# Kernel optimization log

Measured on AMD Instinct MI355X. Metric: run time of the kernel, lower is better.

Reference implementation:

```python
import jax, jax.numpy as jnp
import numpy as np

S, B, C, H, W = 5, 128, 256, 11, 11
HEADS, R, NITER = 8, 2, 2
HD = C // HEADS
SCALE = C ** (-0.5)
EPS = 1e-5


def conv(x, w, b, p=1):
    o = jax.lax.conv_general_dilated(x, w, (1, 1), [(p, p), (p, p)],
                                     dimension_numbers=('NCHW', 'OIHW', 'NCHW'))
    return o + b[None, :, None, None]


def ln(x, g, b):
    # torch LayerNorm over normalized_shape=[C,H,W]
    m = jnp.mean(x, axis=(1, 2, 3), keepdims=True)
    v = jnp.var(x, axis=(1, 2, 3), keepdims=True)
    return (x - m) * jax.lax.rsqrt(v + EPS) * g[None] + b[None]


def setup_inputs():
    ks = iter(jax.random.split(jax.random.key(0), 40))
    def nrm(shp, s=0.02):
        return jax.random.normal(next(ks), shp, jnp.float32) * s
    def c3(o, i):
        return nrm((o, i, 3, 3)), jnp.zeros((o,), jnp.float32)
    d = {}
    d['x'] = jax.random.normal(next(ks), (S, B, C, H, W), jnp.float32)
    d['ing'] = jnp.ones((C, H, W), jnp.float32); d['inb'] = jnp.zeros((C, H, W), jnp.float32)
    d['iqw'], d['iqb'] = c3(C, C); d['ikw'], d['ikb'] = c3(C, C); d['ivw'], d['ivb'] = c3(C, C)
    d['iow'], d['iob'] = c3(C, C)
    d['iong'] = jnp.ones((C, H, W), jnp.float32); d['ionb'] = jnp.zeros((C, H, W), jnp.float32)
    d['ia'] = jnp.array(1.0, jnp.float32)
    d['eng'] = jnp.ones((C, H, W), jnp.float32); d['enb'] = jnp.zeros((C, H, W), jnp.float32)
    d['rpe'] = nrm((2 * R, 1, H, W), 1.0)
    d['mw'], d['mb'] = c3(C, C + 3)  # hidden + 2 temporal + 1 spatial embedding channel
    d['eqw'], d['eqb'] = c3(C, C); d['ekw'], d['ekb'] = c3(C, C); d['evw'], d['evb'] = c3(C, C)
    d['gw'] = nrm((C, 2 * C, 1, 1)); d['gb'] = jnp.zeros((C,), jnp.float32)
    d['eow'], d['eob'] = c3(C, C)
    d['eong'] = jnp.ones((C, H, W), jnp.float32); d['eonb'] = jnp.zeros((C, H, W), jnp.float32)
    d['iia'] = jnp.array(0.5, jnp.float32)
    d['zrw'], d['zrb'] = c3(2 * C, 2 * C)
    d['hw_'], d['hb_'] = c3(C, 2 * C)
    d['ng'] = jnp.ones((C, H, W), jnp.float32); d['nb'] = jnp.zeros((C, H, W), jnp.float32)
    return d


def _forward(x, ing, inb, iqw, iqb, ikw, ikb, ivw, ivb, iow, iob, iong, ionb, ia,
             eng, enb, rpe, mw, mb, eqw, eqb, ekw, ekb, evw, evb, gw, gb,
             eow, eob, eong, eonb, iia, zrw, zrb, hw_, hb_, ng, nb):
    def intra_all(h):
        # intra-frame self-attention, vectorized over all S frames at once
        xf = h.reshape(S * B, C, H, W)
        xn = ln(xf, ing, inb)
        q = conv(xn, iqw, iqb).reshape(S * B, C, H * W)
        k = conv(xn, ikw, ikb).reshape(S * B, C, H * W)
        v = conv(xn, ivw, ivb).reshape(S * B, C, H * W)
        a = jax.nn.softmax(jnp.einsum('bcn,bcm->bnm', q, k) * SCALE, axis=-1)
        o = jnp.einsum('bnm,bcm->bcn', a, v).reshape(S * B, C, H, W)
        o = jax.nn.relu(ln(conv(o, iow, iob), iong, ionb))
        return (ia * o + xn).reshape(S, B, C, H, W)

    def inter_one(i, h):
        xn = ln(h[i], eng, enb)
        q = conv(xn, eqw, eqb).reshape(B, HEADS, HD, H * W)
        out = jnp.zeros((B, C, H, W), jnp.float32)
        for j in range(S):
            if j == i or abs(i - j) > R:
                continue
            idx = (i - j + R - 1) % (2 * R)  # mimics python negative indexing in torch
            tenc = jnp.array([1.0 if i < j else -1.0, abs(i - j) / R], jnp.float32)
            tenc = jnp.broadcast_to(tenc[None, :, None, None], (B, 2, H, W))
            sp = jnp.broadcast_to(rpe[idx][None], (B, 1, H, W))
            y = conv(jnp.concatenate([h[j], tenc, sp], axis=1), mw, mb)
            k = conv(y, ekw, ekb).reshape(B, HEADS, HD, H * W)
            v = conv(y, evw, evb).reshape(B, HEADS, HD, H * W)
            a = jax.nn.softmax(jnp.einsum('bhdn,bhdm->bhnm', q, k) * SCALE, axis=-1)
            msg = jnp.einsum('bhdm,bhnm->bhdn', v, a).reshape(B, C, H, W)
            msg = jax.nn.relu(ln(conv(msg, eow, eob), eong, eonb))
            gate = jax.nn.sigmoid(jnp.mean(conv(jnp.concatenate([xn, msg], axis=1), gw, gb, p=0),
                                           axis=(2, 3), keepdims=True))
            out = out + msg * gate
        return out

    def gru(xin, hprev):
        zr = jax.nn.sigmoid(conv(jnp.concatenate([xin, hprev], axis=1), zrw, zrb))
        z, r = zr[:, :C], zr[:, C:]
        hhat = jnp.tanh(conv(jnp.concatenate([xin, r * hprev], axis=1), hw_, hb_))
        return (1 - z) * hprev + z * hhat

    h = x
    for _ in range(NITER):
        hi = intra_all(h)
        new_h = []
        for i in range(S):
            inter = inter_one(i, h)
            comb = iia * hi[i] + (1 - iia) * inter
            nh = gru(comb, h[i]) + h[i]
            new_h.append(ln(nh, ng, nb))
        h = jnp.stack(new_h, axis=0)
    return h


def reference(x, ing, inb, iqw, iqb, ikw, ikb, ivw, ivb, iow, iob, iong, ionb, ia,
              eng, enb, rpe, mw, mb, eqw, eqb, ekw, ekb, evw, evb, gw, gb,
              eow, eob, eong, eonb, iia, zrw, zrb, hw_, hb_, ng, nb):
    return _forward(x, ing, inb, iqw, iqb, ikw, ikb, ivw, ivb, iow, iob, iong, ionb, ia,
                    eng, enb, rpe, mw, mb, eqw, eqb, ekw, ekb, evw, evb, gw, gb,
                    eow, eob, eong, eonb, iia, zrw, zrb, hw_, hb_, ng, nb)
```

## Files before the change

kernel.cpp:

```cpp
#include <hip/hip_runtime.h>
#include <cstdint>
#include <cstddef>
#include <cmath>


#define Sn 5
#define Bn 128
#define Cn 256
#define Nn 121
#define HEADSn 8
#define NITERn 2
#define EPSf 1e-5f
#define SCALEf 0.0625f
#define CHWn (Cn*Nn)

static const size_t SLICEsz = (size_t)Bn*CHWn;
static const size_t FULLsz  = (size_t)Sn*SLICEsz;
static const size_t SLA     = SLICEsz + 1024;

typedef __attribute__((ext_vector_type(8))) short short8;
typedef __attribute__((ext_vector_type(4))) float f32x4;

static __device__ __forceinline__ short f2bf(float f){
  union { float f; unsigned u; } x; x.f = f;
  unsigned r = (x.u + 0x7FFFu + ((x.u >> 16) & 1u)) >> 16;
  return (short)r;
}

__global__ __launch_bounds__(128) void wprep_kernel(
    const float* __restrict__ w, short* __restrict__ o, int Cin, int Cinp)
{
  const int co = blockIdx.x, tap = blockIdx.y;
  const int G = Cinp >> 7;
  const int coH = co >> 6, ms = (co >> 4) & 3, l15 = co & 15;
  const float* wrow = w + (size_t)co*Cin*9 + tap;
  short* obase = o + (size_t)coH*G*73728 + (size_t)tap*8192 + ms*512 + l15*8;
  for (int ci = threadIdx.x; ci < Cinp; ci += 128){
    const int grp = ci >> 7, kc = (ci >> 5) & 3, quad = (ci >> 3) & 3, e = ci & 7;
    const short val = (ci < Cin) ? f2bf(wrow[(size_t)ci*9]) : (short)0;
    obase[(size_t)grp*73728 + kc*2048 + quad*128 + e] = val;
  }
}

__global__ __launch_bounds__(256) void gwt_kernel(
    const float* __restrict__ gw, float* __restrict__ gwT)
{
  const int k = blockIdx.x, c = threadIdx.x;
  gwT[(size_t)k*256 + c] = gw[(size_t)c*512 + k];
}

__global__ __launch_bounds__(512) void conv_mfma_kernel(
    const float* __restrict__ inA, const float* __restrict__ inA1,
    const float* __restrict__ inB,
    int cinA, int Cin, int Cinp, int Cout,
    const short* __restrict__ wbf, const float* __restrict__ bias,
    float* __restrict__ out,
    int mMode, float4 tcs,
    const float* __restrict__ rp0, const float* __restrict__ rp1)
{
  __shared__ short Xs[128*136];
  const int samp = blockIdx.x;
  const int coB  = blockIdx.y * 128;
  const int t    = threadIdx.x;
  const int lane = t & 63;
  const int wv   = t >> 6;
  const int wy   = wv >> 2;
  const int wx   = wv & 3;
  const int l15  = lane & 15;
  const int quad = lane >> 4;
  const int G    = Cinp >> 7;

  const int pr = samp >> 7;
  const float* baseA = inA1 ? ((pr ? inA1 : inA) + (size_t)(samp & 127)*cinA*Nn)
                            : (inA + (size_t)samp*(size_t)cinA*Nn);
  const float* baseB = inB ? inB + (size_t)samp*(size_t)(Cin-cinA)*Nn : nullptr;
  const float mtc0 = pr ? tcs.z : tcs.x;
  const float mtc1 = pr ? tcs.w : tcs.y;
  const float* rp  = pr ? rp1 : rp0;

  int nout[2], py[2], pxx[2];
  #pragma unroll
  for (int ns = 0; ns < 2; ++ns){
    nout[ns] = wx*32 + ns*16 + l15;
    py[ns]  = nout[ns] / 11;
    pxx[ns] = nout[ns] % 11;
  }

  f32x4 acc[4][2];
  #pragma unroll
  for (int ms = 0; ms < 4; ++ms)
    #pragma unroll
    for (int ns = 0; ns < 2; ++ns) acc[ms][ns] = (f32x4){0.f,0.f,0.f,0.f};

  const short* wgbase = wbf + (size_t)(blockIdx.y*2 + wy)*G*73728 + lane*8;

  const int ngrp = (Cin + 127) >> 7;
  for (int grp = 0; grp < ngrp; ++grp){
    __syncthreads();
    for (int e = t; e < 128*128; e += 512){
      const int px = e & 127, cil = e >> 7;
      const int ci = grp*128 + cil;
      float v = 0.f;
      if (px < Nn && ci < Cin){
        if (mMode && ci >= 256)
          v = (ci == 256) ? mtc0 : (ci == 257) ? mtc1 : rp[px];
        else if (ci < cinA) v = baseA[(size_t)ci*Nn + px];
        else                v = baseB[(size_t)(ci-cinA)*Nn + px];
      }
      Xs[px*136 + cil] = f2bf(v);
    }
    __syncthreads();

    const int rem = Cin - grp*128;
    const short* wgrp = wgbase + (size_t)grp*73728;

    if (rem >= 128){
      for (int tap = 0; tap < 9; ++tap){
        const int dy = tap/3 - 1, dx = tap%3 - 1;
        int pp[2];
        #pragma unroll
        for (int ns = 0; ns < 2; ++ns){
          const int yy = py[ns] + dy, xx = pxx[ns] + dx;
          const bool ok = (nout[ns] < Nn) && yy >= 0 && yy < 11 && xx >= 0 && xx < 11;
          pp[ns] = ok ? yy*11 + xx : Nn;
        }
        const short* wb = wgrp + tap*8192;
        #pragma unroll
        for (int kc = 0; kc < 4; ++kc){
          short8 a[4], b[2];
          #pragma unroll
          for (int ms = 0; ms < 4; ++ms)
            a[ms] = *(const short8*)(wb + kc*2048 + ms*512);
          #pragma unroll
          for (int ns = 0; ns < 2; ++ns)
            b[ns] = *(const short8*)(&Xs[pp[ns]*136 + kc*32 + quad*8]);
          #pragma unroll
          for (int ms = 0; ms < 4; ++ms)
            #pragma unroll
            for (int ns = 0; ns < 2; ++ns)
              acc[ms][ns] = __builtin_amdgcn_mfma_f32_16x16x32_bf16(
                                a[ms], b[ns], acc[ms][ns], 0, 0, 0);
        }
      }
    } else {
      const int nkc = (rem + 31) >> 5;
      for (int tap = 0; tap < 9; ++tap){
        const int dy = tap/3 - 1, dx = tap%3 - 1;
        int pp[2];
        #pragma unroll
        for (int ns = 0; ns < 2; ++ns){
          const int yy = py[ns] + dy, xx = pxx[ns] + dx;
          const bool ok = (nout[ns] < Nn) && yy >= 0 && yy < 11 && xx >= 0 && xx < 11;
          pp[ns] = ok ? yy*11 + xx : Nn;
        }
        const short* wb = wgrp + tap*8192;
        for (int kc = 0; kc < nkc; ++kc){
          short8 a[4], b[2];
          #pragma unroll
          for (int ms = 0; ms < 4; ++ms)
            a[ms] = *(const short8*)(wb + kc*2048 + ms*512);
          #pragma unroll
          for (int ns = 0; ns < 2; ++ns)
            b[ns] = *(const short8*)(&Xs[pp[ns]*136 + kc*32 + quad*8]);
          #pragma unroll
          for (int ms = 0; ms < 4; ++ms)
            #pragma unroll
            for (int ns = 0; ns < 2; ++ns)
              acc[ms][ns] = __builtin_amdgcn_mfma_f32_16x16x32_bf16(
                                a[ms], b[ns], acc[ms][ns], 0, 0, 0);
        }
      }
    }
  }

  #pragma unroll
  for (int ms = 0; ms < 4; ++ms)
    #pragma unroll
    for (int ns = 0; ns < 2; ++ns){
      const int n = nout[ns];
      if (n < Nn){
        const int mbase = coB + wy*64 + ms*16 + quad*4;
        #pragma unroll
        for (int r = 0; r < 4; ++r)
          out[((size_t)samp*Cout + mbase + r)*Nn + n] = acc[ms][ns][r] + bias[mbase + r];
      }
    }
}

__global__ __launch_bounds__(256) void ln_kernel(
    const float* __restrict__ x, const float* __restrict__ g, const float* __restrict__ bb,
    float* __restrict__ out, const float* __restrict__ alpha,
    const float* __restrict__ addend, int relu)
{
  const size_t base = (size_t)blockIdx.x * CHWn;
  const f32x4* xs = (const f32x4*)(x + base);
  const int NV = CHWn/4;
  float sum = 0.f, ss = 0.f;
  for (int i = threadIdx.x; i < NV; i += 256){
    f32x4 v = xs[i];
    sum += v.x + v.y + v.z + v.w;
    ss  += v.x*v.x + v.y*v.y + v.z*v.z + v.w*v.w;
  }
  #pragma unroll
  for (int o = 32; o > 0; o >>= 1){ sum += __shfl_down(sum, o, 64); ss += __shfl_down(ss, o, 64); }
  __shared__ float r1[4], r2[4];
  const int wid = threadIdx.x >> 6;
  if ((threadIdx.x & 63) == 0){ r1[wid] = sum; r2[wid] = ss; }
  __syncthreads();
  sum = r1[0]+r1[1]+r1[2]+r1[3];
  ss  = r2[0]+r2[1]+r2[2]+r2[3];
  const float mean = sum * (1.f/CHWn);
  const float var  = ss * (1.f/CHWn) - mean*mean;
  const float inv  = rsqrtf(var + EPSf);
  const float a = alpha ? *alpha : 1.f;
  const f32x4* gv = (const f32x4*)g;
  const f32x4* bv = (const f32x4*)bb;
  const f32x4* av = addend ? (const f32x4*)(addend + base) : nullptr;
  f32x4* ov = (f32x4*)(out + base);
  for (int i = threadIdx.x; i < NV; i += 256){
    f32x4 v = (xs[i] - mean) * inv * gv[i] + bv[i];
    if (relu){ v.x=fmaxf(v.x,0.f); v.y=fmaxf(v.y,0.f); v.z=fmaxf(v.z,0.f); v.w=fmaxf(v.w,0.f); }
    v *= a;
    if (av) v += av[i];
    ov[i] = v;
  }
}

template<int HDt, int CPT, int NPASS>
__global__ __launch_bounds__(256) void attn_kernel(
    const float* __restrict__ q, const float* __restrict__ k, const float* __restrict__ v,
    float* __restrict__ o, int qs, int ks, int os, int qm)
{
  __shared__ float T[Nn*132];
  const int nh_ = Cn / HDt;
  const int samp = blockIdx.x / nh_;
  const int hh = blockIdx.x % nh_;
  const size_t qoff  = ((size_t)(samp & qm)*qs + hh*HDt)*Nn;
  const size_t kvoff = ((size_t)samp*ks + hh*HDt)*Nn;
  const size_t ooff  = ((size_t)samp*os + hh*HDt)*Nn;
  const int t = threadIdx.x;
  {
    const int tn = t >> 4, tm = t & 15;
    const int n0 = tn*8, m0 = tm*8;
    float acc[8][8];
    #pragma unroll
    for (int a2=0;a2<8;a2++)
      #pragma unroll
      for (int b2=0;b2<8;b2++) acc[a2][b2] = 0.f;
    const float* qp = q + qoff + n0;
    const float* kp = k + kvoff + m0;
    #pragma unroll 2
    for (int d=0; d<HDt; ++d){
      float qv[8], kv[8];
      #pragma unroll
      for (int j2=0;j2<8;j2++){ qv[j2] = qp[d*Nn + j2]; kv[j2] = kp[d*Nn + j2]; }
      #pragma unroll
      for (int a2=0;a2<8;a2++)
        #pragma unroll
        for (int b2=0;b2<8;b2++) acc[a2][b2] = fmaf(qv[a2], kv[b2], acc[a2][b2]);
    }
    #pragma unroll
    for (int b2=0;b2<8;b2++){
      const int m = m0 + b2;
      if (m < Nn){
        #pragma unroll
        for (int a2=0;a2<8;a2++) T[m*132 + n0 + a2] = acc[a2][b2] * SCALEf;
      }
    }
  }
  __syncthreads();
  if (t < Nn){
    float mx = -1e30f;
    for (int m2=0;m2<Nn;m2++) mx = fmaxf(mx, T[m2*132+t]);
    float sum = 0.f;
    for (int m2=0;m2<Nn;m2++){ float e = __expf(T[m2*132+t]-mx); sum += e; T[m2*132+t] = e; }
    const float invs = 1.f/sum;
    for (int m2=0;m2<Nn;m2++) T[m2*132+t] *= invs;
  }
  __syncthreads();
  {
    const int ng_ = t & 15, cg = t >> 4;
    const int an0 = ng_*8;
    for (int pass=0; pass<NPASS; ++pass){
      const int c0 = pass*64 + cg*CPT;
      float av[CPT][8];
      #pragma unroll
      for (int ci2=0;ci2<CPT;ci2++)
        #pragma unroll
        for (int j2=0;j2<8;j2++) av[ci2][j2] = 0.f;
      for (int m2=0;m2<Nn;m2++){
        float tv[8];
        #pragma unroll
        for (int j2=0;j2<8;j2++) tv[j2] = T[m2*132 + an0 + j2];
        #pragma unroll
        for (int ci2=0;ci2<CPT;ci2++){
          const float vv = v[kvoff + (size_t)(c0+ci2)*Nn + m2];
          #pragma unroll
          for (int j2=0;j2<8;j2++) av[ci2][j2] = fmaf(vv, tv[j2], av[ci2][j2]);
        }
      }
      #pragma unroll
      for (int ci2=0;ci2<CPT;ci2++){
        float* op = o + ooff + (size_t)(c0+ci2)*Nn + an0;
        #pragma unroll
        for (int j2=0;j2<8;j2++) if (an0+j2 < Nn) op[j2] = av[ci2][j2];
      }
    }
  }
}

__global__ __launch_bounds__(128) void mean_kernel(const float* __restrict__ x, float* __restrict__ out)
{
  const int s = blockIdx.x; const int c0 = blockIdx.y*8;
  __shared__ float r[2];
  for (int cc=0; cc<8; ++cc){
    const int c = c0+cc;
    float v = 0.f;
    if (threadIdx.x < Nn) v = x[((size_t)s*Cn + c)*Nn + threadIdx.x];
    #pragma unroll
    for (int o=32;o>0;o>>=1) v += __shfl_down(v, o, 64);
    if ((threadIdx.x & 63) == 0) r[threadIdx.x>>6] = v;
    __syncthreads();
    if (threadIdx.x == 0) out[(size_t)s*Cn + c] = (r[0]+r[1]) * (1.f/Nn);
    __syncthreads();
  }
}

__global__ __launch_bounds__(256) void gate_kernel(
    const float* __restrict__ meanX, const float* __restrict__ meanM,
    const float* __restrict__ gwT, const float* __restrict__ gb,
    float* __restrict__ gate, int xm)
{
  const int b = blockIdx.x;
  __shared__ float mv[512];
  mv[threadIdx.x]     = meanX[(size_t)(b & xm)*Cn + threadIdx.x];
  mv[256+threadIdx.x] = meanM[(size_t)b*Cn + threadIdx.x];
  __syncthreads();
  float acc = gb[threadIdx.x];
  for (int k2=0;k2<512;k2++) acc = fmaf(gwT[(size_t)k2*256 + threadIdx.x], mv[k2], acc);
  gate[(size_t)b*Cn + threadIdx.x] = 1.f/(1.f+__expf(-acc));
}

__global__ __launch_bounds__(256) void accum_kernel(
    const float* __restrict__ msg, const float* __restrict__ gate,
    float* __restrict__ outs, int init)
{
  const size_t idx = (size_t)blockIdx.x*256 + threadIdx.x;
  if (idx >= SLICEsz) return;
  const size_t t_ = idx / Nn;
  const int c = (int)(t_ & 255);
  const int b = (int)(t_ >> 8);
  const float v = msg[idx] * gate[(size_t)b*Cn + c];
  outs[idx] = init ? v : (outs[idx] + v);
}

__global__ __launch_bounds__(256) void comb_kernel(float* __restrict__ hi,
    const float* __restrict__ outi, const float* __restrict__ iia)
{
  const size_t idx = (size_t)blockIdx.x*256 + threadIdx.x;
  if (idx >= SLICEsz) return;
  const float a = *iia;
  hi[idx] = a*hi[idx] + (1.f-a)*outi[idx];
}

__global__ __launch_bounds__(256) void rh_kernel(const float* __restrict__ zrq,
    const float* __restrict__ h, float* __restrict__ rh, size_t nelem)
{
  const size_t idx = (size_t)blockIdx.x*256 + threadIdx.x;
  if (idx >= nelem) return;
  const int n_ = (int)(idx % Nn);
  const size_t t_ = idx / Nn;
  const int c = (int)(t_ & 255);
  const size_t s = t_ >> 8;
  float r = zrq[(s*512 + 256 + c)*Nn + n_];
  r = 1.f/(1.f+__expf(-r));
  rh[idx] = r*h[idx];
}

__global__ __launch_bounds__(256) void nh_kernel(const float* __restrict__ zrq,
    const float* __restrict__ hq, const float* __restrict__ h,
    float* __restrict__ nh, size_t nelem)
{
  const size_t idx = (size_t)blockIdx.x*256 + threadIdx.x;
  if (idx >= nelem) return;
  const int n_ = (int)(idx % Nn);
  const size_t t_ = idx / Nn;
  const int c = (int)(t_ & 255);
  const size_t s = t_ >> 8;
  float z = zrq[(s*512 + c)*Nn + n_];
  z = 1.f/(1.f+__expf(-z));
  const float hv = h[idx];
  nh[idx] = (1.f-z)*hv + z*tanhf(hq[idx]) + hv;
}

static const int PJ[5][4] = {{1,2,0,0},{0,2,3,0},{0,1,3,4},{1,2,4,0},{2,3,0,0}};
static const int PNP[5]   = {2,3,4,3,2};

extern "C" void kernel_launch(void* const* d_in, const int* in_sizes, int n_in,
                              void* d_out, int out_size, void* d_ws, size_t ws_size,
                              hipStream_t stream)
{
  (void)in_sizes; (void)n_in; (void)out_size;
  const float* x   = (const float*)d_in[0];
  const float* ing = (const float*)d_in[1];
  const float* inb = (const float*)d_in[2];
  const float* iqw = (const float*)d_in[3];
  const float* iqb = (const float*)d_in[4];
  const float* ikw = (const float*)d_in[5];
  const float* ikb = (const float*)d_in[6];
  const float* ivw = (const float*)d_in[7];
  const float* ivb = (const float*)d_in[8];
  const float* iow = (const float*)d_in[9];
  const float* iob = (const float*)d_in[10];
  const float* iong= (const float*)d_in[11];
  const float* ionb= (const float*)d_in[12];
  const float* ia  = (const float*)d_in[13];
  const float* eng = (const float*)d_in[14];
  const float* enb = (const float*)d_in[15];
  const float* rpe = (const float*)d_in[16];
  const float* mw  = (const float*)d_in[17];
  const float* mb  = (const float*)d_in[18];
  const float* eqw = (const float*)d_in[19];
  const float* eqb = (const float*)d_in[20];
  const float* ekw = (const float*)d_in[21];
  const float* ekb = (const float*)d_in[22];
  const float* evw = (const float*)d_in[23];
  const float* evb = (const float*)d_in[24];
  const float* gw  = (const float*)d_in[25];
  const float* gb  = (const float*)d_in[26];
  const float* eow = (const float*)d_in[27];
  const float* eob = (const float*)d_in[28];
  const float* eong= (const float*)d_in[29];
  const float* eonb= (const float*)d_in[30];
  const float* iia = (const float*)d_in[31];
  const float* zrw = (const float*)d_in[32];
  const float* zrb = (const float*)d_in[33];
  const float* hww = (const float*)d_in[34];
  const float* hwb = (const float*)d_in[35];
  const float* ng  = (const float*)d_in[36];
  const float* nbg = (const float*)d_in[37];

  float* W = (float*)d_ws;
  size_t off = 0;
  float* h      = W + off; off += FULLsz + 1024;
  float* big    = W + off; off += 6*SLICEsz + 1024;
  float* p2     = W + off; off += 2*SLICEsz + 1024;
  float* xsl    = W + off; off += 2*SLICEsz + 1024;
  float* qsl    = W + off; off += SLA;
  float* osl    = W + off; off += SLA;
  float* meanXb = W + off; off += Bn*Cn;
  float* meanM  = W + off; off += 2*Bn*Cn;
  float* gateb  = W + off; off += 2*Bn*Cn;
  float* bqkv   = W + off; off += 768;
  float* bekv   = W + off; off += 512;
  float* gwT    = W + off; off += 512*256;
  short* WB = (short*)(W + off);
  size_t so = 0;
  short* iqB = WB + so; so += (size_t)256*9*256;
  short* ikB = WB + so; so += (size_t)256*9*256;
  short* ivB = WB + so; so += (size_t)256*9*256;
  short* ioB = WB + so; so += (size_t)256*9*256;
  short* eqB = WB + so; so += (size_t)256*9*256;
  short* ekB = WB + so; so += (size_t)256*9*256;
  short* evB = WB + so; so += (size_t)256*9*256;
  short* eoB = WB + so; so += (size_t)256*9*256;
  short* mB_ = WB + so; so += (size_t)256*9*384;
  short* zrB = WB + so; so += (size_t)512*9*512;
  short* hwB = WB + so; so += (size_t)256*9*512;
  off += (so + 1) / 2;
  if (ws_size < off * sizeof(float)) return;

  float* hi = (float*)d_out;

  hipMemcpyAsync(h, x, FULLsz*sizeof(float), hipMemcpyDeviceToDevice, stream);
  hipMemcpyAsync(bqkv,     iqb, 256*sizeof(float), hipMemcpyDeviceToDevice, stream);
  hipMemcpyAsync(bqkv+256, ikb, 256*sizeof(float), hipMemcpyDeviceToDevice, stream);
  hipMemcpyAsync(bqkv+512, ivb, 256*sizeof(float), hipMemcpyDeviceToDevice, stream);
  hipMemcpyAsync(bekv,     ekb, 256*sizeof(float), hipMemcpyDeviceToDevice, stream);
  hipMemcpyAsync(bekv+256, evb, 256*sizeof(float), hipMemcpyDeviceToDevice, stream);

  wprep_kernel<<<dim3(256,9),128,0,stream>>>(iqw, iqB, 256, 256);
  wprep_kernel<<<dim3(256,9),128,0,stream>>>(ikw, ikB, 256, 256);
  wprep_kernel<<<dim3(256,9),128,0,stream>>>(ivw, ivB, 256, 256);
  wprep_kernel<<<dim3(256,9),128,0,stream>>>(iow, ioB, 256, 256);
  wprep_kernel<<<dim3(256,9),128,0,stream>>>(eqw, eqB, 256, 256);
  wprep_kernel<<<dim3(256,9),128,0,stream>>>(ekw, ekB, 256, 256);
  wprep_kernel<<<dim3(256,9),128,0,stream>>>(evw, evB, 256, 256);
  wprep_kernel<<<dim3(256,9),128,0,stream>>>(eow, eoB, 256, 256);
  wprep_kernel<<<dim3(256,9),128,0,stream>>>(mw,  mB_, 259, 384);
  wprep_kernel<<<dim3(512,9),128,0,stream>>>(zrw, zrB, 512, 512);
  wprep_kernel<<<dim3(256,9),128,0,stream>>>(hww, hwB, 512, 512);
  gwt_kernel<<<512,256,0,stream>>>(gw, gwT);

  const int gridSlc = (int)(SLICEsz / 256);
  const float4 f4z = {0.f,0.f,0.f,0.f};

  #define CONV(inA_, inB_, Cin_, Cinp_, Cout_, wb_, bi_, out_, NS_)              \
    conv_mfma_kernel<<<dim3(Bn*(NS_), (Cout_)/128), 512, 0, stream>>>(           \
        inA_, nullptr, inB_, 256, Cin_, Cinp_, Cout_, wb_, bi_, out_,            \
        0, f4z, nullptr, nullptr)

  for (int it = 0; it < NITERn; ++it){
    for (int s0 = 0; s0 < Sn; s0 += 2){
      const int cn = (Sn - s0 >= 2) ? 2 : 1;
      const float* hs = h + (size_t)s0*SLICEsz;
      ln_kernel<<<Bn*cn,256,0,stream>>>(hs, ing, inb, xsl, nullptr, nullptr, 0);
      CONV(xsl, nullptr, 256, 256, 768, iqB, bqkv, big, cn);
      attn_kernel<256,4,4><<<Bn*cn,256,0,stream>>>(big, big + (size_t)256*Nn,
                                                big + (size_t)512*Nn, p2,
                                                768, 768, 256, 0x7fffffff);
      CONV(p2, nullptr, 256, 256, 256, ioB, iob, big, cn);
      ln_kernel<<<Bn*cn,256,0,stream>>>(big, iong, ionb, hi + (size_t)s0*SLICEsz, ia, xsl, 1);
    }

    for (int i = 0; i < Sn; ++i){
      ln_kernel<<<Bn,256,0,stream>>>(h + (size_t)i*SLICEsz, eng, enb, xsl, nullptr, nullptr, 0);
      CONV(xsl, nullptr, 256, 256, 256, eqB, eqb, qsl, 1);
      mean_kernel<<<dim3(Bn,32),128,0,stream>>>(xsl, meanXb);
      const int np = PNP[i];
      int done = 0; int first = 1;
      while (done < np){
        const int cn = (np - done >= 2) ? 2 : 1;
        const int j0 = PJ[i][done];
        const int j1 = PJ[i][done + cn - 1];
        const float4 tcs = { (i < j0) ? 1.f : -1.f, fabsf((float)(i - j0)) * 0.5f,
                             (i < j1) ? 1.f : -1.f, fabsf((float)(i - j1)) * 0.5f };
        const int r0 = (((i - j0 + 1) % 4) + 4) % 4;
        const int r1 = (((i - j1 + 1) % 4) + 4) % 4;
        conv_mfma_kernel<<<dim3(Bn*cn,2),512,0,stream>>>(
            h + (size_t)j0*SLICEsz, h + (size_t)j1*SLICEsz, nullptr,
            256, 259, 384, 256, mB_, mb, big,
            1, tcs, rpe + (size_t)r0*Nn, rpe + (size_t)r1*Nn);
        CONV(big, nullptr, 256, 256, 512, ekB, bekv, big + 2*SLICEsz, cn);
        attn_kernel<32,2,1><<<Bn*cn*HEADSn,256,0,stream>>>(
            qsl, big + 2*SLICEsz, big + 2*SLICEsz + (size_t)256*Nn, big,
            256, 512, 256, 127);
        CONV(big, nullptr, 256, 256, 256, eoB, eob, p2, cn);
        ln_kernel<<<Bn*cn,256,0,stream>>>(p2, eong, eonb, p2, nullptr, nullptr, 1);
        mean_kernel<<<dim3(Bn*cn,32),128,0,stream>>>(p2, meanM);
        gate_kernel<<<Bn*cn,256,0,stream>>>(meanXb, meanM, gwT, gb, gateb, 127);
        accum_kernel<<<gridSlc,256,0,stream>>>(p2, gateb, osl, first);
        if (cn == 2)
          accum_kernel<<<gridSlc,256,0,stream>>>(p2 + SLICEsz, gateb + Bn*Cn, osl, 0);
        first = 0; done += cn;
      }
      comb_kernel<<<gridSlc,256,0,stream>>>(hi + (size_t)i*SLICEsz, osl, iia);
    }

    for (int s0 = 0; s0 < Sn; s0 += 2){
      const int cn = (Sn - s0 >= 2) ? 2 : 1;
      const float* hs = h + (size_t)s0*SLICEsz;
      float* cs = hi + (size_t)s0*SLICEsz;
      CONV(cs, hs, 512, 512, 512, zrB, zrb, big, cn);
      rh_kernel<<<gridSlc*cn,256,0,stream>>>(big, hs, xsl, (size_t)cn*SLICEsz);
      CONV(cs, xsl, 512, 512, 256, hwB, hwb, p2, cn);
      nh_kernel<<<gridSlc*cn,256,0,stream>>>(big, p2, hs, xsl, (size_t)cn*SLICEsz);
      float* dst = (it == NITERn-1) ? cs : (float*)hs;
      ln_kernel<<<Bn*cn,256,0,stream>>>(xsl, ng, nbg, dst, nullptr, nullptr, 0);
    }
  }
  #undef CONV
}
```

Baseline: 14.25 ms.

## Batch inter-frame pairs across frames in fixed pairs, fold comb into accumulate

```diff
diff --git a/kernel.cpp b/kernel.cpp
--- a/kernel.cpp
+++ b/kernel.cpp
@@ -16,7 +16,6 @@
 
 static const size_t SLICEsz = (size_t)Bn*CHWn;
 static const size_t FULLsz  = (size_t)Sn*SLICEsz;
-static const size_t SLA     = SLICEsz + 1024;
 
 typedef __attribute__((ext_vector_type(8))) short short8;
 typedef __attribute__((ext_vector_type(4))) float f32x4;
@@ -229,13 +228,18 @@
 template<int HDt, int CPT, int NPASS>
 __global__ __launch_bounds__(256) void attn_kernel(
     const float* __restrict__ q, const float* __restrict__ k, const float* __restrict__ v,
-    float* __restrict__ o, int qs, int ks, int os, int qm)
+    float* __restrict__ o, int qs, int ks, int os, int qsel0, int qsel1)
 {
   __shared__ float T[Nn*132];
   const int nh_ = Cn / HDt;
   const int samp = blockIdx.x / nh_;
   const int hh = blockIdx.x % nh_;
-  const size_t qoff  = ((size_t)(samp & qm)*qs + hh*HDt)*Nn;
+  size_t qoff;
+  if (qsel0 < 0) qoff = ((size_t)samp*qs + hh*HDt)*Nn;
+  else {
+    const int slot = (samp >> 7) ? qsel1 : qsel0;
+    qoff = ((size_t)slot*Bn + (samp & 127))*(size_t)CHWn + (size_t)hh*HDt*Nn;
+  }
   const size_t kvoff = ((size_t)samp*ks + hh*HDt)*Nn;
   const size_t ooff  = ((size_t)samp*os + hh*HDt)*Nn;
   const int t = threadIdx.x;
@@ -329,11 +333,12 @@
 __global__ __launch_bounds__(256) void gate_kernel(
     const float* __restrict__ meanX, const float* __restrict__ meanM,
     const float* __restrict__ gwT, const float* __restrict__ gb,
-    float* __restrict__ gate, int xm)
+    float* __restrict__ gate, int xi0, int xi1)
 {
   const int b = blockIdx.x;
+  const int xi = (b >> 7) ? xi1 : xi0;
   __shared__ float mv[512];
-  mv[threadIdx.x]     = meanX[(size_t)(b & xm)*Cn + threadIdx.x];
+  mv[threadIdx.x]     = meanX[((size_t)xi*Bn + (b & 127))*Cn + threadIdx.x];
   mv[256+threadIdx.x] = meanM[(size_t)b*Cn + threadIdx.x];
   __syncthreads();
   float acc = gb[threadIdx.x];
@@ -343,24 +348,16 @@
 
 __global__ __launch_bounds__(256) void accum_kernel(
     const float* __restrict__ msg, const float* __restrict__ gate,
-    float* __restrict__ outs, int init)
+    float* __restrict__ hi, const float* __restrict__ iia, int init)
 {
   const size_t idx = (size_t)blockIdx.x*256 + threadIdx.x;
   if (idx >= SLICEsz) return;
   const size_t t_ = idx / Nn;
   const int c = (int)(t_ & 255);
   const int b = (int)(t_ >> 8);
-  const float v = msg[idx] * gate[(size_t)b*Cn + c];
-  outs[idx] = init ? v : (outs[idx] + v);
-}
-
-__global__ __launch_bounds__(256) void comb_kernel(float* __restrict__ hi,
-    const float* __restrict__ outi, const float* __restrict__ iia)
-{
-  const size_t idx = (size_t)blockIdx.x*256 + threadIdx.x;
-  if (idx >= SLICEsz) return;
   const float a = *iia;
-  hi[idx] = a*hi[idx] + (1.f-a)*outi[idx];
+  const float w = (1.f - a) * msg[idx] * gate[(size_t)b*Cn + c];
+  hi[idx] = init ? (a*hi[idx] + w) : (hi[idx] + w);
 }
 
 __global__ __launch_bounds__(256) void rh_kernel(const float* __restrict__ zrq,
@@ -393,8 +390,9 @@
   nh[idx] = (1.f-z)*hv + z*tanhf(hq[idx]) + hv;
 }
 
-static const int PJ[5][4] = {{1,2,0,0},{0,2,3,0},{0,1,3,4},{1,2,4,0},{2,3,0,0}};
-static const int PNP[5]   = {2,3,4,3,2};
+static const int PIg[14] = {0,0,1,1,1,2,2,2,2,3,3,3,4,4};
+static const int PJg[14] = {1,2,0,2,3,0,1,3,4,1,2,4,2,3};
+static const int FIRSTP[5] = {0,2,5,9,12};
 
 extern "C" void kernel_launch(void* const* d_in, const int* in_sizes, int n_in,
                               void* d_out, int out_size, void* d_ws, size_t ws_size,
@@ -446,9 +444,8 @@
   float* big    = W + off; off += 6*SLICEsz + 1024;
   float* p2     = W + off; off += 2*SLICEsz + 1024;
   float* xsl    = W + off; off += 2*SLICEsz + 1024;
-  float* qsl    = W + off; off += SLA;
-  float* osl    = W + off; off += SLA;
-  float* meanXb = W + off; off += Bn*Cn;
+  float* qsl    = W + off; off += 2*SLICEsz + 1024;
+  float* meanXb = W + off; off += 2*Bn*Cn;
   float* meanM  = W + off; off += 2*Bn*Cn;
   float* gateb  = W + off; off += 2*Bn*Cn;
   float* bqkv   = W + off; off += 768;
@@ -500,6 +497,16 @@
         inA_, nullptr, inB_, 256, Cin_, Cinp_, Cout_, wb_, bi_, out_,            \
         0, f4z, nullptr, nullptr)
 
+  #define PREAMBLE(i_, cn_)                                                      \
+    do {                                                                          \
+      ln_kernel<<<Bn*(cn_),256,0,stream>>>(h + (size_t)(i_)*SLICEsz, eng, enb,    \
+                                           xsl, nullptr, nullptr, 0);             \
+      CONV(xsl, nullptr, 256, 256, 256, eqB, eqb,                                 \
+           qsl + (size_t)((i_)&1)*SLICEsz, cn_);                                  \
+      mean_kernel<<<dim3(Bn*(cn_),32),128,0,stream>>>(xsl,                        \
+           meanXb + (size_t)((i_)&1)*Bn*Cn);                                      \
+    } while (0)
+
   for (int it = 0; it < NITERn; ++it){
     for (int s0 = 0; s0 < Sn; s0 += 2){
       const int cn = (Sn - s0 >= 2) ? 2 : 1;
@@ -508,43 +515,40 @@
       CONV(xsl, nullptr, 256, 256, 768, iqB, bqkv, big, cn);
       attn_kernel<256,4,4><<<Bn*cn,256,0,stream>>>(big, big + (size_t)256*Nn,
                                                 big + (size_t)512*Nn, p2,
-                                                768, 768, 256, 0x7fffffff);
+                                                768, 768, 256, -1, -1);
       CONV(p2, nullptr, 256, 256, 256, ioB, iob, big, cn);
       ln_kernel<<<Bn*cn,256,0,stream>>>(big, iong, ionb, hi + (size_t)s0*SLICEsz, ia, xsl, 1);
     }
 
-    for (int i = 0; i < Sn; ++i){
-      ln_kernel<<<Bn,256,0,stream>>>(h + (size_t)i*SLICEsz, eng, enb, xsl, nullptr, nullptr, 0);
-      CONV(xsl, nullptr, 256, 256, 256, eqB, eqb, qsl, 1);
-      mean_kernel<<<dim3(Bn,32),128,0,stream>>>(xsl, meanXb);
-      const int np = PNP[i];
-      int done = 0; int first = 1;
-      while (done < np){
-        const int cn = (np - done >= 2) ? 2 : 1;
-        const int j0 = PJ[i][done];
-        const int j1 = PJ[i][done + cn - 1];
-        const float4 tcs = { (i < j0) ? 1.f : -1.f, fabsf((float)(i - j0)) * 0.5f,
-                             (i < j1) ? 1.f : -1.f, fabsf((float)(i - j1)) * 0.5f };
-        const int r0 = (((i - j0 + 1) % 4) + 4) % 4;
-        const int r1 = (((i - j1 + 1) % 4) + 4) % 4;
-        conv_mfma_kernel<<<dim3(Bn*cn,2),512,0,stream>>>(
-            h + (size_t)j0*SLICEsz, h + (size_t)j1*SLICEsz, nullptr,
-            256, 259, 384, 256, mB_, mb, big,
-            1, tcs, rpe + (size_t)r0*Nn, rpe + (size_t)r1*Nn);
-        CONV(big, nullptr, 256, 256, 512, ekB, bekv, big + 2*SLICEsz, cn);
-        attn_kernel<32,2,1><<<Bn*cn*HEADSn,256,0,stream>>>(
-            qsl, big + 2*SLICEsz, big + 2*SLICEsz + (size_t)256*Nn, big,
-            256, 512, 256, 127);
-        CONV(big, nullptr, 256, 256, 256, eoB, eob, p2, cn);
-        ln_kernel<<<Bn*cn,256,0,stream>>>(p2, eong, eonb, p2, nullptr, nullptr, 1);
-        mean_kernel<<<dim3(Bn*cn,32),128,0,stream>>>(p2, meanM);
-        gate_kernel<<<Bn*cn,256,0,stream>>>(meanXb, meanM, gwT, gb, gateb, 127);
-        accum_kernel<<<gridSlc,256,0,stream>>>(p2, gateb, osl, first);
-        if (cn == 2)
-          accum_kernel<<<gridSlc,256,0,stream>>>(p2 + SLICEsz, gateb + Bn*Cn, osl, 0);
-        first = 0; done += cn;
-      }
-      comb_kernel<<<gridSlc,256,0,stream>>>(hi + (size_t)i*SLICEsz, osl, iia);
+    for (int c = 0; c < 7; ++c){
+      if (c == 0) PREAMBLE(0, 2);
+      if (c == 2) PREAMBLE(2, 1);
+      if (c == 4) PREAMBLE(3, 1);
+      if (c == 6) PREAMBLE(4, 1);
+
+      const int p0 = 2*c, p1 = 2*c + 1;
+      const int i0 = PIg[p0], j0 = PJg[p0];
+      const int i1 = PIg[p1], j1 = PJg[p1];
+      const float4 tcs = { (i0 < j0) ? 1.f : -1.f, fabsf((float)(i0 - j0)) * 0.5f,
+                           (i1 < j1) ? 1.f : -1.f, fabsf((float)(i1 - j1)) * 0.5f };
+      const int r0 = (((i0 - j0 + 1) % 4) + 4) % 4;
+      const int r1 = (((i1 - j1 + 1) % 4) + 4) % 4;
+      conv_mfma_kernel<<<dim3(Bn*2,2),512,0,stream>>>(
+          h + (size_t)j0*SLICEsz, h + (size_t)j1*SLICEsz, nullptr,
+          256, 259, 384, 256, mB_, mb, big,
+          1, tcs, rpe + (size_t)r0*Nn, rpe + (size_t)r1*Nn);
+      CONV(big, nullptr, 256, 256, 512, ekB, bekv, big + 2*SLICEsz, 2);
+      attn_kernel<32,2,1><<<Bn*2*HEADSn,256,0,stream>>>(
+          qsl, big + 2*SLICEsz, big + 2*SLICEsz + (size_t)256*Nn, big,
+          256, 512, 256, i0 & 1, i1 & 1);
+      CONV(big, nullptr, 256, 256, 256, eoB, eob, p2, 2);
+      ln_kernel<<<Bn*2,256,0,stream>>>(p2, eong, eonb, p2, nullptr, nullptr, 1);
+      mean_kernel<<<dim3(Bn*2,32),128,0,stream>>>(p2, meanM);
+      gate_kernel<<<Bn*2,256,0,stream>>>(meanXb, meanM, gwT, gb, gateb, i0 & 1, i1 & 1);
+      accum_kernel<<<gridSlc,256,0,stream>>>(p2, gateb,
+          hi + (size_t)i0*SLICEsz, iia, p0 == FIRSTP[i0]);
+      accum_kernel<<<gridSlc,256,0,stream>>>(p2 + SLICEsz, gateb + Bn*Cn,
+          hi + (size_t)i1*SLICEsz, iia, p1 == FIRSTP[i1]);
     }
 
     for (int s0 = 0; s0 < Sn; s0 += 2){
@@ -559,5 +563,6 @@
       ln_kernel<<<Bn*cn,256,0,stream>>>(xsl, ng, nbg, dst, nullptr, nullptr, 0);
     }
   }
+  #undef PREAMBLE
   #undef CONV
 }
```

Result: faster. 13.73 ms (-3.7%).
